# Kernel optimization log

Hardware: AMD Instinct MI355X
Metric: run time of the kernel (lower is better)

## Reference

```python
import jax, jax.numpy as jnp
import numpy as np
import math

NUM_HEADS = 16
NUM_KV_HEADS = 4
HEAD_DIM = 128
ROPE_THETA = 10000.0


def _rope(x, cos, sin):
    # x: [b, h, s, d]; cos/sin: [1, 1, s, d//2]
    half = x.shape[-1] // 2
    x1, x2 = x[..., :half], x[..., half:]
    return jnp.concatenate([x1 * cos - x2 * sin, x2 * cos + x1 * sin], axis=-1)


def setup_inputs() -> dict:
    key = jax.random.key(0)
    ks = jax.random.split(key, 5)
    B, S, H = 2, 2048, 2048
    scale_qk = (2.0 / (H + H)) ** 0.5
    scale_kv = (2.0 / (H + NUM_KV_HEADS * HEAD_DIM)) ** 0.5
    return {
        "hidden_states": jax.random.normal(ks[0], (B, S, H), jnp.float32),
        "Wq": jax.random.normal(ks[1], (NUM_HEADS * HEAD_DIM, H), jnp.float32) * scale_qk,
        "Wk": jax.random.normal(ks[2], (NUM_KV_HEADS * HEAD_DIM, H), jnp.float32) * scale_kv,
        "Wv": jax.random.normal(ks[3], (NUM_KV_HEADS * HEAD_DIM, H), jnp.float32) * scale_kv,
        "Wo": jax.random.normal(ks[4], (NUM_HEADS * HEAD_DIM, H), jnp.float32) * scale_qk,
    }


def reference(hidden_states, Wq, Wk, Wv, Wo):
    B, S, H = hidden_states.shape
    hd = HEAD_DIM

    q = (hidden_states @ Wq.T).reshape(B, S, NUM_HEADS, hd).transpose(0, 2, 1, 3)
    k = (hidden_states @ Wk.T).reshape(B, S, NUM_KV_HEADS, hd).transpose(0, 2, 1, 3)
    v = (hidden_states @ Wv.T).reshape(B, S, NUM_KV_HEADS, hd).transpose(0, 2, 1, 3)

    # RoPE (half-split variant, as in module)
    inv_freq = 1.0 / (ROPE_THETA ** (jnp.arange(0, hd, 2, dtype=jnp.float32) / hd))
    pos = jnp.arange(S, dtype=jnp.float32)
    freqs = pos[:, None] * inv_freq[None, :]           # [S, hd//2]
    cos = jnp.cos(freqs)[None, None]                   # [1,1,S,hd//2]
    sin = jnp.sin(freqs)[None, None]
    q = _rope(q, cos, sin)
    k = _rope(k, cos, sin)

    # GQA: repeat kv heads (repeat_interleave semantics)
    n_rep = NUM_HEADS // NUM_KV_HEADS
    k = jnp.repeat(k, n_rep, axis=1)
    v = jnp.repeat(v, n_rep, axis=1)

    scores = jnp.einsum("bhqd,bhkd->bhqk", q, k) / math.sqrt(hd)
    attn = jax.nn.softmax(scores, axis=-1)
    out = jnp.einsum("bhqk,bhkd->bhqd", attn, v)
    out = out.transpose(0, 2, 1, 3).reshape(B, S, NUM_HEADS * hd)
    return out @ Wo.T
```

## Files before the change

kernel.cpp:

```cpp
#include <hip/hip_runtime.h>
#include <cstdint>
#include <cstddef>

typedef __bf16 bf16x8 __attribute__((ext_vector_type(8)));
typedef __bf16 bf16x4 __attribute__((ext_vector_type(4)));
typedef float  f32x4  __attribute__((ext_vector_type(4)));

__device__ __forceinline__ void gload_lds16(const void* g, void* l) {
    __builtin_amdgcn_global_load_lds(
        (const __attribute__((address_space(1))) void*)g,
        (__attribute__((address_space(3))) void*)l, 16, 0, 0);
}

#define VM6B asm volatile("s_waitcnt vmcnt(6) lgkmcnt(0)\ns_barrier" ::: "memory")
#define VM4B asm volatile("s_waitcnt vmcnt(4) lgkmcnt(0)\ns_barrier" ::: "memory")
#define VM0B asm volatile("s_waitcnt vmcnt(0) lgkmcnt(0)\ns_barrier" ::: "memory")
#define BARO asm volatile("s_barrier" ::: "memory")
#define WAITB4 asm volatile("s_waitcnt vmcnt(4) lgkmcnt(0)\ns_barrier" ::: "memory")
#define WAITB0 asm volatile("s_waitcnt vmcnt(0) lgkmcnt(0)\ns_barrier" ::: "memory")

#define SEQ 2048
#define NH 16
#define NKV 4
#define HD 128

__global__ __launch_bounds__(256) void cvt_all(const float* __restrict__ hs,
                                               const float* __restrict__ wq,
                                               const float* __restrict__ wk,
                                               const float* __restrict__ wv,
                                               const float* __restrict__ wo,
                                               __bf16* __restrict__ hB,
                                               __bf16* __restrict__ WqkB,
                                               __bf16* __restrict__ WvB,
                                               __bf16* __restrict__ WoB) {
    int bid = blockIdx.x;
    const float* in; __bf16* out; int base;
    if (bid < 8192)        { in = hs; out = hB;                   base = bid; }
    else if (bid < 12288)  { in = wq; out = WqkB;                 base = bid - 8192; }
    else if (bid < 13312)  { in = wk; out = WqkB + 2048 * 2048;   base = bid - 12288; }
    else if (bid < 14336)  { in = wv; out = WvB;                  base = bid - 13312; }
    else                   { in = wo; out = WoB;                  base = bid - 14336; }
    int i = base * 256 + threadIdx.x;
    float4 v = ((const float4*)in)[i];
    bf16x4 o = { (__bf16)v.x, (__bf16)v.y, (__bf16)v.z, (__bf16)v.w };
    ((bf16x4*)out)[i] = o;
}

__device__ __forceinline__ void stage_half(const __bf16* __restrict__ M,
                                           char* dbuf, int bmn, int k0, int half,
                                           int wave, int lane) {
    char* hb = dbuf + (half & 1) * 32768 + (half >> 1) * 16384;
    int kbase = k0 + (half >> 1) * 32;
#pragma unroll
    for (int g = 0; g < 2; ++g) {
        int c = wave * 2 + g;
        int row = (c & 3) * 64 + lane;
        int ks = c >> 2;
        gload_lds16(M + (size_t)(bmn + row) * 2048 + kbase + ks * 8, hb + c * 1024);
    }
}

template <int KS, int MH>
__device__ __forceinline__ void phase_mfma(const __bf16* bA, const __bf16* bB,
                                           int quad, int l16, int wr128, int colbase,
                                           bf16x8 (&bq)[4], f32x4 acc[8][4]) {
    bf16x8 af[4];
#pragma unroll
    for (int ii = 0; ii < 4; ++ii)
        af[ii] = *(const bf16x8*)(bA + (KS * 4 + quad) * 2048 +
                                  (wr128 + (MH * 4 + ii) * 16 + l16) * 8);
    if (MH == 0) {
#pragma unroll
        for (int j = 0; j < 4; ++j)
            bq[j] = *(const bf16x8*)(bB + (KS * 4 + quad) * 2048 +
                                     (colbase + (j & 1) * 16 + (j >> 1) * 64 + l16) * 8);
    }
    __builtin_amdgcn_s_setprio(1);
#pragma unroll
    for (int ii = 0; ii < 4; ++ii)
#pragma unroll
        for (int j = 0; j < 4; ++j)
            acc[MH * 4 + ii][j] = __builtin_amdgcn_mfma_f32_16x16x32_bf16(
                af[ii], bq[j], acc[MH * 4 + ii][j], 0, 0, 0);
    __builtin_amdgcn_s_setprio(0);
}

__device__ __forceinline__ void gemm_core(const __bf16* __restrict__ A,
                                          const __bf16* __restrict__ B,
                                          char* lds, int bm, int bn,
                                          int wave, int lane, int quad, int l16,
                                          int wr128, int colbase, f32x4 acc[8][4]) {
    const int NT = 32;
    stage_half(A, lds, bm, 0, 0, wave, lane);
    stage_half(B, lds, bn, 0, 1, wave, lane);
    stage_half(A, lds, bm, 0, 2, wave, lane);
    stage_half(B, lds, bn, 0, 3, wave, lane);
    int cur = 0;
    for (int t = 0; t < NT - 1; ++t) {
        const __bf16* bA = (const __bf16*)(lds + cur * 65536);
        const __bf16* bB = (const __bf16*)(lds + cur * 65536 + 32768);
        char* nb = lds + (cur ^ 1) * 65536;
        int k1 = (t + 1) * 64;
        bf16x8 bq[4];
        stage_half(A, nb, bm, k1, 0, wave, lane);
        VM6B;
        phase_mfma<0, 0>(bA, bB, quad, l16, wr128, colbase, bq, acc);
        stage_half(B, nb, bn, k1, 1, wave, lane);
        BARO;
        phase_mfma<0, 1>(bA, bB, quad, l16, wr128, colbase, bq, acc);
        stage_half(A, nb, bm, k1, 2, wave, lane);
        VM6B;
        phase_mfma<1, 0>(bA, bB, quad, l16, wr128, colbase, bq, acc);
        stage_half(B, nb, bn, k1, 3, wave, lane);
        BARO;
        phase_mfma<1, 1>(bA, bB, quad, l16, wr128, colbase, bq, acc);
        cur ^= 1;
    }
    {
        const __bf16* bA = (const __bf16*)(lds + cur * 65536);
        const __bf16* bB = (const __bf16*)(lds + cur * 65536 + 32768);
        bf16x8 bq[4];
        VM4B;
        phase_mfma<0, 0>(bA, bB, quad, l16, wr128, colbase, bq, acc);
        phase_mfma<0, 1>(bA, bB, quad, l16, wr128, colbase, bq, acc);
        VM0B;
        phase_mfma<1, 0>(bA, bB, quad, l16, wr128, colbase, bq, acc);
        phase_mfma<1, 1>(bA, bB, quad, l16, wr128, colbase, bq, acc);
    }
}

__global__ __launch_bounds__(512, 2) void qkv_gemm(const __bf16* __restrict__ hB,
                                                   const __bf16* __restrict__ Wqk,
                                                   const __bf16* __restrict__ Wv,
                                                   __bf16* __restrict__ Qr,
                                                   __bf16* __restrict__ Kr,
                                                   __bf16* __restrict__ VT) {
    __shared__ __align__(16) char lds[2 * 65536];
    const int tid = threadIdx.x;
    const int wave = tid >> 6, lane = tid & 63;
    const int quad = lane >> 4, l16 = lane & 15;
    const int wr = wave >> 2, wc = wave & 3;
    const int x = blockIdx.x, y = blockIdx.y;
    const bool isVT = (y >= 10);
    const bool isQ = (y < 8);

    const __bf16* Amat = isVT ? Wv : hB;
    const __bf16* Bmat = isVT ? hB : (isQ ? Wqk : Wqk + 2048 * 2048);
    const int bm = isVT ? (y - 10) * 256 : x * 256;
    const int bn = isVT ? x * 256 : (isQ ? y * 256 : (y - 8) * 256);

    const int wr128 = wr * 128;
    const int colbase = (wc >> 1) * 128 + (wc & 1) * 32;

    f32x4 acc[8][4] = {};
    gemm_core(Amat, Bmat, lds, bm, bn, wave, lane, quad, l16, wr128, colbase, acc);

    if (isVT) {
#pragma unroll
        for (int i = 0; i < 8; ++i)
#pragma unroll
            for (int j = 0; j < 4; ++j) {
                int row = bm + wr128 + i * 16 + quad * 4;
                int col = bn + colbase + (j & 1) * 16 + (j >> 1) * 64 + l16;
#pragma unroll
                for (int r = 0; r < 4; ++r)
                    VT[(size_t)(row + r) * 4096 + col] = (__bf16)acc[i][j][r];
            }
    } else {
        __bf16* outp = isQ ? Qr : Kr;
        const float sc = isQ ? 0.08838834764831845f : 1.0f;
        const int nh = isQ ? NH : NKV;
        const int hh = (isQ ? y * 2 : (y - 8) * 2) + (wc >> 1);
#pragma unroll
        for (int j2 = 0; j2 < 2; ++j2) {
            int d = (wc & 1) * 32 + j2 * 16 + l16;
            float inv = exp2f(-(float)d * 0.2076205059304601f);
#pragma unroll
            for (int i = 0; i < 8; ++i)
#pragma unroll
                for (int r = 0; r < 4; ++r) {
                    int m = bm + wr128 + i * 16 + quad * 4 + r;
                    int s = m & (SEQ - 1), b = m >> 11;
                    float f = (float)s * inv;
                    float c = __cosf(f) * sc, sn = __sinf(f) * sc;
                    float x1 = acc[i][j2][r], x2 = acc[i][j2 + 2][r];
                    size_t rb = ((size_t)(b * nh + hh) * SEQ + s) * HD;
                    outp[rb + d]      = (__bf16)(x1 * c - x2 * sn);
                    outp[rb + d + 64] = (__bf16)(x2 * c + x1 * sn);
                }
        }
    }
}

__global__ __launch_bounds__(512, 2) void gemm_bt_f32(const __bf16* __restrict__ A,
                                                      const __bf16* __restrict__ W,
                                                      float* __restrict__ C) {
    __shared__ __align__(16) char lds[2 * 65536];
    const int tid = threadIdx.x;
    const int wave = tid >> 6, lane = tid & 63;
    const int quad = lane >> 4, l16 = lane & 15;
    const int wr = wave >> 2, wc = wave & 3;
    const int bm = blockIdx.x * 256, bn = blockIdx.y * 256;
    const int wr128 = wr * 128;
    const int colbase = (wc >> 1) * 128 + (wc & 1) * 32;

    f32x4 acc[8][4] = {};
    gemm_core(A, W, lds, bm, bn, wave, lane, quad, l16, wr128, colbase, acc);

#pragma unroll
    for (int i = 0; i < 8; ++i)
#pragma unroll
        for (int j = 0; j < 4; ++j) {
            int row = bm + wr128 + i * 16 + quad * 4;
            int col = bn + colbase + (j & 1) * 16 + (j >> 1) * 64 + l16;
#pragma unroll
            for (int r = 0; r < 4; ++r)
                C[(size_t)(row + r) * 2048 + col] = acc[i][j][r];
        }
}

__global__ __launch_bounds__(512, 1) void attn_kernel(const __bf16* __restrict__ Q,
                                                      const __bf16* __restrict__ Kr,
                                                      const __bf16* __restrict__ VT,
                                                      __bf16* __restrict__ AO) {
    __shared__ __align__(16) char ring[3 * 32768];
    __shared__ __align__(16) __bf16 Pb[8][32][72];

    const int tid = threadIdx.x;
    const int wave = tid >> 6, lane = tid & 63;
    const int quad = lane >> 4, l16 = lane & 15;
    const int h = blockIdx.y, b = blockIdx.z;
    const int kv = h >> 2;
    const int qbase = blockIdx.x * 256 + wave * 32;

    bf16x8 qf[2][4];
#pragma unroll
    for (int qs = 0; qs < 2; ++qs) {
        const __bf16* Qp =
            Q + ((size_t)(b * NH + h) * SEQ + qbase + qs * 16 + l16) * HD + quad * 8;
#pragma unroll
        for (int kq = 0; kq < 4; ++kq) qf[qs][kq] = *(const bf16x8*)(Qp + kq * 32);
    }

    const __bf16* Kp = Kr + (size_t)(b * NKV + kv) * SEQ * HD;
    const __bf16* Vp = VT + (size_t)(kv * HD) * (2 * SEQ) + b * SEQ;

    f32x4 oacc[2][8] = {};
    float lpart[2] = {0.f, 0.f};

    auto stage = [&](int sb, int k0) {
        char* dst = ring + sb * 32768;
#pragma unroll
        for (int tt = 0; tt < 4; ++tt) {
            int c = wave * 4 + tt;
            if (c < 16) {
                gload_lds16(Kp + (size_t)(k0 + lane) * HD + c * 8, dst + c * 1024);
            } else {
                int vc = c - 16;
                gload_lds16(Vp + (size_t)(((vc & 1) << 6) + lane) * (2 * SEQ) + k0 +
                                (vc >> 1) * 8,
                            dst + c * 1024);
            }
        }
    };

    auto compute = [&](int cb) {
        const __bf16* kt = (const __bf16*)(ring + cb * 32768);
        const __bf16* vt = kt + 8192;
#pragma unroll
        for (int mt = 0; mt < 4; ++mt) {
            f32x4 s0 = {0.f, 0.f, 0.f, 0.f}, s1 = {0.f, 0.f, 0.f, 0.f};
#pragma unroll
            for (int kq = 0; kq < 4; ++kq) {
                bf16x8 ka = *(const bf16x8*)(kt + (kq * 4 + quad) * 512 +
                                             (mt * 16 + l16) * 8);
                s0 = __builtin_amdgcn_mfma_f32_16x16x32_bf16(ka, qf[0][kq], s0, 0, 0, 0);
                s1 = __builtin_amdgcn_mfma_f32_16x16x32_bf16(ka, qf[1][kq], s1, 0, 0, 0);
            }
            bf16x4 pk0, pk1;
#pragma unroll
            for (int r = 0; r < 4; ++r) {
                float p0 = __expf(s0[r]);
                float p1 = __expf(s1[r]);
                lpart[0] += p0; lpart[1] += p1;
                pk0[r] = (__bf16)p0; pk1[r] = (__bf16)p1;
            }
            *(bf16x4*)&Pb[wave][l16][mt * 16 + quad * 4] = pk0;
            *(bf16x4*)&Pb[wave][16 + l16][mt * 16 + quad * 4] = pk1;
        }
#pragma unroll
        for (int kk = 0; kk < 2; ++kk) {
            bf16x8 pb0 = *(const bf16x8*)&Pb[wave][l16][kk * 32 + quad * 8];
            bf16x8 pb1 = *(const bf16x8*)&Pb[wave][16 + l16][kk * 32 + quad * 8];
#pragma unroll
            for (int mt = 0; mt < 8; ++mt) {
                bf16x8 va = *(const bf16x8*)(vt + (kk * 4 + quad) * 1024 +
                                             (mt * 16 + l16) * 8);
                oacc[0][mt] = __builtin_amdgcn_mfma_f32_16x16x32_bf16(
                    va, pb0, oacc[0][mt], 0, 0, 0);
                oacc[1][mt] = __builtin_amdgcn_mfma_f32_16x16x32_bf16(
                    va, pb1, oacc[1][mt], 0, 0, 0);
            }
        }
    };

    stage(0, 0);
    stage(1, 64);

    int cb = 0;
    for (int t = 0; t < 31; ++t) {
        WAITB4;
        if (t < 30) {
            int sb = cb + 2; if (sb >= 3) sb -= 3;
            stage(sb, (t + 2) * 64);
        }
        compute(cb);
        if (++cb == 3) cb = 0;
    }
    WAITB0;
    compute(cb);

#pragma unroll
    for (int qs = 0; qs < 2; ++qs) {
        lpart[qs] += __shfl_xor(lpart[qs], 16);
        lpart[qs] += __shfl_xor(lpart[qs], 32);
        float inv = 1.f / lpart[qs];
        int q = qbase + qs * 16 + l16;
#pragma unroll
        for (int mt = 0; mt < 8; ++mt) {
            bf16x4 ov;
#pragma unroll
            for (int r = 0; r < 4; ++r) ov[r] = (__bf16)(oacc[qs][mt][r] * inv);
            *(bf16x4*)(AO + ((size_t)(b * SEQ + q)) * (NH * HD) + h * HD +
                       mt * 16 + quad * 4) = ov;
        }
    }
}

extern "C" void kernel_launch(void* const* d_in, const int* in_sizes, int n_in,
                              void* d_out, int out_size, void* d_ws, size_t ws_size,
                              hipStream_t stream) {
    const float* hs = (const float*)d_in[0];
    const float* Wq = (const float*)d_in[1];
    const float* Wk = (const float*)d_in[2];
    const float* Wv = (const float*)d_in[3];
    const float* Wo = (const float*)d_in[4];
    float* out = (float*)d_out;
    char* ws = (char*)d_ws;

    __bf16* Qr   = (__bf16*)(ws + 0);
    __bf16* Kr   = (__bf16*)(ws + 16777216);
    __bf16* VT   = (__bf16*)(ws + 20971520);
    __bf16* WoB  = (__bf16*)(ws + 25165824);
    __bf16* hB   = (__bf16*)(ws + 33554432);
    __bf16* WqkB = (__bf16*)(ws + 50331648);
    __bf16* WvB  = (__bf16*)(ws + 60817408);
    __bf16* AO   = (__bf16*)(ws + 33554432);

    cvt_all<<<18432, 256, 0, stream>>>(hs, Wq, Wk, Wv, Wo, hB, WqkB, WvB, WoB);

    qkv_gemm<<<dim3(16, 12), 512, 0, stream>>>(hB, WqkB, WvB, Qr, Kr, VT);

    attn_kernel<<<dim3(8, 16, 2), 512, 0, stream>>>(Qr, Kr, VT, AO);

    gemm_bt_f32<<<dim3(16, 8), 512, 0, stream>>>(AO, WoB, out);
}
```

Baseline: 361.7 us.

## Retile attention and output GEMM, add XCD-aware block remapping

Attention now runs 256-thread blocks over 128 queries with 32-key tiles and a smaller LDS ring, which doubles the grid and allows two blocks per CU. The output projection GEMM now uses 128x256 tiles with its own triple-buffered pipeline and MFMA priority hints, giving 256 blocks instead of 128. All three kernels remap block IDs so that consecutive tiles land on the same XCD, aiming at better L2 reuse. The trade-off is more loop iterations and barriers per block, with less work in each.

```diff
diff --git a/kernel.cpp b/kernel.cpp
--- a/kernel.cpp
+++ b/kernel.cpp
@@ -140,7 +140,9 @@
     const int wave = tid >> 6, lane = tid & 63;
     const int quad = lane >> 4, l16 = lane & 15;
     const int wr = wave >> 2, wc = wave & 3;
-    const int x = blockIdx.x, y = blockIdx.y;
+    int wg = blockIdx.y * 16 + blockIdx.x;
+    wg = (wg & 7) * 24 + (wg >> 3);
+    const int x = wg & 15, y = wg >> 4;
     const bool isVT = (y >= 10);
     const bool isQ = (y < 8);
 
@@ -192,46 +194,105 @@
     }
 }
 
-__global__ __launch_bounds__(512, 2) void gemm_bt_f32(const __bf16* __restrict__ A,
+__global__ __launch_bounds__(512, 1) void gemm_bt_f32(const __bf16* __restrict__ A,
                                                       const __bf16* __restrict__ W,
                                                       float* __restrict__ C) {
-    __shared__ __align__(16) char lds[2 * 65536];
+    __shared__ __align__(16) char lds[3 * 49152];
     const int tid = threadIdx.x;
     const int wave = tid >> 6, lane = tid & 63;
     const int quad = lane >> 4, l16 = lane & 15;
     const int wr = wave >> 2, wc = wave & 3;
-    const int bm = blockIdx.x * 256, bn = blockIdx.y * 256;
-    const int wr128 = wr * 128;
-    const int colbase = (wc >> 1) * 128 + (wc & 1) * 32;
-
-    f32x4 acc[8][4] = {};
-    gemm_core(A, W, lds, bm, bn, wave, lane, quad, l16, wr128, colbase, acc);
-
-#pragma unroll
-    for (int i = 0; i < 8; ++i)
+    int wg = blockIdx.y * 32 + blockIdx.x;
+    wg = (wg & 7) * 32 + (wg >> 3);
+    const int bm = (wg & 31) * 128, bn = (wg >> 5) * 256;
+
+    f32x4 acc[4][4] = {};
+
+    auto stageT = [&](int sb, int k0) {
+        char* dst = lds + sb * 49152;
+#pragma unroll
+        for (int tt = 0; tt < 6; ++tt) {
+            int c = wave * 6 + tt;
+            if (c < 16) {
+                int row = ((c & 1) << 6) + lane;
+                gload_lds16(A + (size_t)(bm + row) * 2048 + k0 + (c >> 1) * 8,
+                            dst + c * 1024);
+            } else {
+                int vc = c - 16;
+                int row = ((vc & 3) << 6) + lane;
+                gload_lds16(W + (size_t)(bn + row) * 2048 + k0 + (vc >> 2) * 8,
+                            dst + 16384 + vc * 1024);
+            }
+        }
+    };
+
+    auto computeT = [&](int cb2) {
+        const __bf16* bA = (const __bf16*)(lds + cb2 * 49152);
+        const __bf16* bB = bA + 8192;
+#pragma unroll
+        for (int ks = 0; ks < 2; ++ks) {
+            bf16x8 af[4], bq[4];
+#pragma unroll
+            for (int i = 0; i < 4; ++i)
+                af[i] = *(const bf16x8*)(bA + (ks * 4 + quad) * 1024 +
+                                         (wr * 64 + i * 16 + l16) * 8);
+#pragma unroll
+            for (int j = 0; j < 4; ++j)
+                bq[j] = *(const bf16x8*)(bB + (ks * 4 + quad) * 2048 +
+                                         (wc * 64 + j * 16 + l16) * 8);
+            __builtin_amdgcn_s_setprio(1);
+#pragma unroll
+            for (int i = 0; i < 4; ++i)
+#pragma unroll
+                for (int j = 0; j < 4; ++j)
+                    acc[i][j] = __builtin_amdgcn_mfma_f32_16x16x32_bf16(
+                        af[i], bq[j], acc[i][j], 0, 0, 0);
+            __builtin_amdgcn_s_setprio(0);
+        }
+    };
+
+    stageT(0, 0);
+    stageT(1, 64);
+    int cb = 0;
+    for (int t = 0; t < 31; ++t) {
+        VM6B;
+        if (t < 30) {
+            int sb = cb + 2; if (sb >= 3) sb -= 3;
+            stageT(sb, (t + 2) * 64);
+        }
+        computeT(cb);
+        if (++cb == 3) cb = 0;
+    }
+    VM0B;
+    computeT(cb);
+
+#pragma unroll
+    for (int i = 0; i < 4; ++i)
 #pragma unroll
         for (int j = 0; j < 4; ++j) {
-            int row = bm + wr128 + i * 16 + quad * 4;
-            int col = bn + colbase + (j & 1) * 16 + (j >> 1) * 64 + l16;
+            int row = bm + wr * 64 + i * 16 + quad * 4;
+            int col = bn + wc * 64 + j * 16 + l16;
 #pragma unroll
             for (int r = 0; r < 4; ++r)
                 C[(size_t)(row + r) * 2048 + col] = acc[i][j][r];
         }
 }
 
-__global__ __launch_bounds__(512, 1) void attn_kernel(const __bf16* __restrict__ Q,
+__global__ __launch_bounds__(256, 2) void attn_kernel(const __bf16* __restrict__ Q,
                                                       const __bf16* __restrict__ Kr,
                                                       const __bf16* __restrict__ VT,
                                                       __bf16* __restrict__ AO) {
-    __shared__ __align__(16) char ring[3 * 32768];
-    __shared__ __align__(16) __bf16 Pb[8][32][72];
+    __shared__ __align__(16) char ring[3 * 16384];
+    __shared__ __align__(16) __bf16 Pb[4][32][40];
 
     const int tid = threadIdx.x;
     const int wave = tid >> 6, lane = tid & 63;
     const int quad = lane >> 4, l16 = lane & 15;
-    const int h = blockIdx.y, b = blockIdx.z;
+    int wg = (blockIdx.z * 16 + blockIdx.y) * 16 + blockIdx.x;
+    wg = (wg & 7) * 64 + (wg >> 3);
+    const int x = wg & 15, h = (wg >> 4) & 15, b = wg >> 8;
     const int kv = h >> 2;
-    const int qbase = blockIdx.x * 256 + wave * 32;
+    const int qbase = x * 128 + wave * 32;
 
     bf16x8 qf[2][4];
 #pragma unroll
@@ -249,30 +310,32 @@
     float lpart[2] = {0.f, 0.f};
 
     auto stage = [&](int sb, int k0) {
-        char* dst = ring + sb * 32768;
+        char* dst = ring + sb * 16384;
 #pragma unroll
         for (int tt = 0; tt < 4; ++tt) {
             int c = wave * 4 + tt;
-            if (c < 16) {
-                gload_lds16(Kp + (size_t)(k0 + lane) * HD + c * 8, dst + c * 1024);
+            if (c < 8) {
+                gload_lds16(Kp + (size_t)(k0 + (lane & 31)) * HD +
+                                (2 * c + (lane >> 5)) * 8,
+                            dst + c * 1024);
             } else {
-                int vc = c - 16;
+                int vc = c - 8;
                 gload_lds16(Vp + (size_t)(((vc & 1) << 6) + lane) * (2 * SEQ) + k0 +
                                 (vc >> 1) * 8,
-                            dst + c * 1024);
+                            dst + 8192 + vc * 1024);
             }
         }
     };
 
     auto compute = [&](int cb) {
-        const __bf16* kt = (const __bf16*)(ring + cb * 32768);
-        const __bf16* vt = kt + 8192;
-#pragma unroll
-        for (int mt = 0; mt < 4; ++mt) {
+        const __bf16* kt = (const __bf16*)(ring + cb * 16384);
+        const __bf16* vt = kt + 4096;
+#pragma unroll
+        for (int mt = 0; mt < 2; ++mt) {
             f32x4 s0 = {0.f, 0.f, 0.f, 0.f}, s1 = {0.f, 0.f, 0.f, 0.f};
 #pragma unroll
             for (int kq = 0; kq < 4; ++kq) {
-                bf16x8 ka = *(const bf16x8*)(kt + (kq * 4 + quad) * 512 +
+                bf16x8 ka = *(const bf16x8*)(kt + (kq * 4 + quad) * 256 +
                                              (mt * 16 + l16) * 8);
                 s0 = __builtin_amdgcn_mfma_f32_16x16x32_bf16(ka, qf[0][kq], s0, 0, 0, 0);
                 s1 = __builtin_amdgcn_mfma_f32_16x16x32_bf16(ka, qf[1][kq], s1, 0, 0, 0);
@@ -288,31 +351,26 @@
             *(bf16x4*)&Pb[wave][l16][mt * 16 + quad * 4] = pk0;
             *(bf16x4*)&Pb[wave][16 + l16][mt * 16 + quad * 4] = pk1;
         }
-#pragma unroll
-        for (int kk = 0; kk < 2; ++kk) {
-            bf16x8 pb0 = *(const bf16x8*)&Pb[wave][l16][kk * 32 + quad * 8];
-            bf16x8 pb1 = *(const bf16x8*)&Pb[wave][16 + l16][kk * 32 + quad * 8];
-#pragma unroll
-            for (int mt = 0; mt < 8; ++mt) {
-                bf16x8 va = *(const bf16x8*)(vt + (kk * 4 + quad) * 1024 +
-                                             (mt * 16 + l16) * 8);
-                oacc[0][mt] = __builtin_amdgcn_mfma_f32_16x16x32_bf16(
-                    va, pb0, oacc[0][mt], 0, 0, 0);
-                oacc[1][mt] = __builtin_amdgcn_mfma_f32_16x16x32_bf16(
-                    va, pb1, oacc[1][mt], 0, 0, 0);
-            }
+        bf16x8 pb0 = *(const bf16x8*)&Pb[wave][l16][quad * 8];
+        bf16x8 pb1 = *(const bf16x8*)&Pb[wave][16 + l16][quad * 8];
+#pragma unroll
+        for (int mt = 0; mt < 8; ++mt) {
+            bf16x8 va = *(const bf16x8*)(vt + quad * 1024 + (mt * 16 + l16) * 8);
+            oacc[0][mt] = __builtin_amdgcn_mfma_f32_16x16x32_bf16(
+                va, pb0, oacc[0][mt], 0, 0, 0);
+            oacc[1][mt] = __builtin_amdgcn_mfma_f32_16x16x32_bf16(
+                va, pb1, oacc[1][mt], 0, 0, 0);
         }
     };
 
     stage(0, 0);
-    stage(1, 64);
-
+    stage(1, 32);
     int cb = 0;
-    for (int t = 0; t < 31; ++t) {
+    for (int t = 0; t < 63; ++t) {
         WAITB4;
-        if (t < 30) {
+        if (t < 62) {
             int sb = cb + 2; if (sb >= 3) sb -= 3;
-            stage(sb, (t + 2) * 64);
+            stage(sb, (t + 2) * 32);
         }
         compute(cb);
         if (++cb == 3) cb = 0;
@@ -361,7 +419,7 @@
 
     qkv_gemm<<<dim3(16, 12), 512, 0, stream>>>(hB, WqkB, WvB, Qr, Kr, VT);
 
-    attn_kernel<<<dim3(8, 16, 2), 512, 0, stream>>>(Qr, Kr, VT, AO);
-
-    gemm_bt_f32<<<dim3(16, 8), 512, 0, stream>>>(AO, WoB, out);
-}
+    attn_kernel<<<dim3(16, 16, 2), 256, 0, stream>>>(Qr, Kr, VT, AO);
+
+    gemm_bt_f32<<<dim3(32, 8), 512, 0, stream>>>(AO, WoB, out);
+}
```

New measurement: 334.4 us. -7.5%, faster.
